# Kernel tuning notes

Measured on AMD Instinct MI355X. Metric: run time of the kernel, lower is better.

The kernel has to match this reference:

```python
import jax, jax.numpy as jnp
import numpy as np

EPS = 1e-5  # forward() default eps


def setup_inputs() -> dict:
    key = jax.random.key(0)
    k1, k2 = jax.random.split(key)
    x = jax.random.normal(k1, (16, 4, 1024, 1024), dtype=jnp.float32)
    hole = jax.random.uniform(k2, x.shape) < 0.3
    x = jnp.where(hole, 0.0, x)
    return {"x": x}


def reference(x):
    # mask_type='eq', mask_value=0: valid positions are x != 0
    valid = x != 0.0
    v = valid.astype(x.dtype)
    axes = (1, 2, 3)  # per-sample reduction over C,H,W (4D input skips per-channel branch)
    n = jnp.sum(v, axis=axes, keepdims=True)                       # [B,1,1,1] valid counts
    mean = jnp.sum(x * v, axis=axes, keepdims=True) / n            # masked mean
    centered = jnp.where(valid, x - mean, x)                       # masked-out entries unchanged
    # torch.var on the masked subset of the centered values: unbiased (ddof=1)
    m2 = jnp.sum(centered * v, axis=axes, keepdims=True) / n
    var = jnp.sum(v * (centered - m2) ** 2, axis=axes, keepdims=True) / (n - 1.0)
    out = jnp.where(valid, centered / (jnp.sqrt(var) + EPS), x)
    return out
```

## Files before the change

kernel.cpp:

```cpp
#include <hip/hip_runtime.h>


#define EPS 1e-5

typedef float v4f __attribute__((ext_vector_type(4)));

constexpr int B               = 16;
constexpr int VEC_PER_SAMPLE  = 1 << 20;
constexpr int RED_BLOCKS_PS   = 128;
constexpr int RED_THREADS     = 256;
constexpr int RED_VPT         = VEC_PER_SAMPLE / (RED_BLOCKS_PS * RED_THREADS);
constexpr int NORM_THREADS    = 256;
constexpr int NORM_VPT        = 4;
constexpr int NORM_BLOCKS_PS  = VEC_PER_SAMPLE / (NORM_THREADS * NORM_VPT);

constexpr size_t FIN_OFFSET = (size_t)B * RED_BLOCKS_PS * 3 * sizeof(double);

__global__ __launch_bounds__(RED_THREADS)
void masked_stats_kernel(const float4* __restrict__ x, double* __restrict__ part) {
    const int sample = blockIdx.x / RED_BLOCKS_PS;
    const int blk    = blockIdx.x % RED_BLOCKS_PS;
    const float4* xs = x + (size_t)sample * VEC_PER_SAMPLE
                         + (size_t)blk * (RED_THREADS * RED_VPT);

    float s1[4] = {0.f, 0.f, 0.f, 0.f};
    float s2[4] = {0.f, 0.f, 0.f, 0.f};
    int   cn[4] = {0, 0, 0, 0};

    for (int k = 0; k < RED_VPT; k += 4) {
        #pragma unroll
        for (int u = 0; u < 4; ++u) {
            float4 v = xs[(k + u) * RED_THREADS + threadIdx.x];
            s1[u] += (v.x + v.y) + (v.z + v.w);
            s2[u] += v.x * v.x;
            s2[u] += v.y * v.y;
            s2[u] += v.z * v.z;
            s2[u] += v.w * v.w;
            cn[u] += (v.x != 0.0f) + (v.y != 0.0f) + (v.z != 0.0f) + (v.w != 0.0f);
        }
    }

    double d1 = ((double)s1[0] + s1[1]) + ((double)s1[2] + s1[3]);
    double d2 = ((double)s2[0] + s2[1]) + ((double)s2[2] + s2[3]);
    int    ct = (cn[0] + cn[1]) + (cn[2] + cn[3]);

    #pragma unroll
    for (int off = 32; off > 0; off >>= 1) {
        d1 += __shfl_down(d1, off);
        d2 += __shfl_down(d2, off);
        ct += __shfl_down(ct, off);
    }

    __shared__ double L1[4], L2[4];
    __shared__ int    LC[4];
    const int wave = threadIdx.x >> 6;
    if ((threadIdx.x & 63) == 0) { L1[wave] = d1; L2[wave] = d2; LC[wave] = ct; }
    __syncthreads();
    if (threadIdx.x == 0) {
        double t1 = 0.0, t2 = 0.0; int tc = 0;
        #pragma unroll
        for (int w = 0; w < 4; ++w) { t1 += L1[w]; t2 += L2[w]; tc += LC[w]; }
        part[(size_t)blockIdx.x * 3 + 0] = t1;
        part[(size_t)blockIdx.x * 3 + 1] = t2;
        part[(size_t)blockIdx.x * 3 + 2] = (double)tc;
    }
}

__global__ __launch_bounds__(128)
void finalize_stats_kernel(const double* __restrict__ part, float2* __restrict__ fin) {
    const int sample = blockIdx.x;
    const size_t p = ((size_t)sample * RED_BLOCKS_PS + threadIdx.x) * 3;
    double d1 = part[p + 0];
    double d2 = part[p + 1];
    double dc = part[p + 2];

    #pragma unroll
    for (int off = 32; off > 0; off >>= 1) {
        d1 += __shfl_down(d1, off);
        d2 += __shfl_down(d2, off);
        dc += __shfl_down(dc, off);
    }

    __shared__ double L1[2], L2[2], LC[2];
    const int wave = threadIdx.x >> 6;
    if ((threadIdx.x & 63) == 0) { L1[wave] = d1; L2[wave] = d2; LC[wave] = dc; }
    __syncthreads();
    if (threadIdx.x == 0) {
        double S1 = L1[0] + L1[1];
        double S2 = L2[0] + L2[1];
        double n  = LC[0] + LC[1];
        double mean = S1 / n;
        double var  = (S2 - S1 * S1 / n) / (n - 1.0);
        float2 mi;
        mi.x = (float)mean;
        mi.y = (float)(1.0 / (sqrt(var) + EPS));
        fin[sample] = mi;
    }
}

__global__ __launch_bounds__(NORM_THREADS)
void masked_norm_kernel(const float4* __restrict__ x, v4f* __restrict__ out,
                        const float2* __restrict__ fin) {
    const int sample = blockIdx.x / NORM_BLOCKS_PS;
    const int blk    = blockIdx.x % NORM_BLOCKS_PS;
    const float2 mi  = fin[sample];
    const float mean = mi.x, inv = mi.y;

    const size_t base = (size_t)sample * VEC_PER_SAMPLE
                      + (size_t)blk * (NORM_THREADS * NORM_VPT);

    #pragma unroll
    for (int u = 0; u < NORM_VPT; ++u) {
        const size_t idx = base + (size_t)u * NORM_THREADS + threadIdx.x;
        float4 v = x[idx];
        v4f o;
        o.x = (v.x != 0.0f) ? (v.x - mean) * inv : 0.0f;
        o.y = (v.y != 0.0f) ? (v.y - mean) * inv : 0.0f;
        o.z = (v.z != 0.0f) ? (v.z - mean) * inv : 0.0f;
        o.w = (v.w != 0.0f) ? (v.w - mean) * inv : 0.0f;
        __builtin_nontemporal_store(o, &out[idx]);
    }
}

extern "C" void kernel_launch(void* const* d_in, const int* in_sizes, int n_in,
                              void* d_out, int out_size, void* d_ws, size_t ws_size,
                              hipStream_t stream) {
    const float4* x    = (const float4*)d_in[0];
    v4f*          out  = (v4f*)d_out;
    double*       part = (double*)d_ws;
    float2*       fin  = (float2*)((char*)d_ws + FIN_OFFSET);

    masked_stats_kernel<<<B * RED_BLOCKS_PS, RED_THREADS, 0, stream>>>(x, part);
    finalize_stats_kernel<<<B, 128, 0, stream>>>(part, fin);
    masked_norm_kernel<<<B * NORM_BLOCKS_PS, NORM_THREADS, 0, stream>>>(x, out, fin);
}
```

Before: 473.8 us.

## Fuse stats, finalize and normalize into one cooperative kernel with grid sync

Replaces the three-kernel pipeline with a single cooperative kernel. Each block computes partial sums and publishes them with release stores, then a grid-wide sync runs. After the sync each block reduces its sample's partials and normalizes the same chunk it just read. This removes two kernel launches and the intermediate finalize step, and may reuse cached input. In exchange it needs all blocks co-resident and pays a grid barrier.

```diff
diff --git a/kernel.cpp b/kernel.cpp
--- a/kernel.cpp
+++ b/kernel.cpp
@@ -1,36 +1,35 @@
 #include <hip/hip_runtime.h>
+#include <hip/hip_cooperative_groups.h>
 
 
 #define EPS 1e-5
 
 typedef float v4f __attribute__((ext_vector_type(4)));
 
-constexpr int B               = 16;
-constexpr int VEC_PER_SAMPLE  = 1 << 20;
-constexpr int RED_BLOCKS_PS   = 128;
-constexpr int RED_THREADS     = 256;
-constexpr int RED_VPT         = VEC_PER_SAMPLE / (RED_BLOCKS_PS * RED_THREADS);
-constexpr int NORM_THREADS    = 256;
-constexpr int NORM_VPT        = 4;
-constexpr int NORM_BLOCKS_PS  = VEC_PER_SAMPLE / (NORM_THREADS * NORM_VPT);
+constexpr int B              = 16;
+constexpr int VEC_PER_SAMPLE = 1 << 20;
+constexpr int THREADS        = 256;
+constexpr int BLOCKS_PS      = 64;
+constexpr int BLOCKS         = B * BLOCKS_PS;
+constexpr int VPT            = VEC_PER_SAMPLE / (BLOCKS_PS * THREADS);
 
-constexpr size_t FIN_OFFSET = (size_t)B * RED_BLOCKS_PS * 3 * sizeof(double);
-
-__global__ __launch_bounds__(RED_THREADS)
-void masked_stats_kernel(const float4* __restrict__ x, double* __restrict__ part) {
-    const int sample = blockIdx.x / RED_BLOCKS_PS;
-    const int blk    = blockIdx.x % RED_BLOCKS_PS;
-    const float4* xs = x + (size_t)sample * VEC_PER_SAMPLE
-                         + (size_t)blk * (RED_THREADS * RED_VPT);
+__global__ __launch_bounds__(THREADS, 4)
+void fused_masked_norm(const float4* __restrict__ x, v4f* __restrict__ out,
+                       double* __restrict__ part) {
+    const int sample = blockIdx.x / BLOCKS_PS;
+    const int blk    = blockIdx.x % BLOCKS_PS;
+    const size_t base = (size_t)sample * VEC_PER_SAMPLE
+                      + (size_t)blk * (THREADS * VPT);
+    const float4* xs = x + base;
 
     float s1[4] = {0.f, 0.f, 0.f, 0.f};
     float s2[4] = {0.f, 0.f, 0.f, 0.f};
     int   cn[4] = {0, 0, 0, 0};
 
-    for (int k = 0; k < RED_VPT; k += 4) {
+    for (int k = 0; k < VPT; k += 4) {
         #pragma unroll
         for (int u = 0; u < 4; ++u) {
-            float4 v = xs[(k + u) * RED_THREADS + threadIdx.x];
+            float4 v = xs[(k + u) * THREADS + threadIdx.x];
             s1[u] += (v.x + v.y) + (v.z + v.w);
             s2[u] += v.x * v.x;
             s2[u] += v.y * v.y;
@@ -57,68 +56,55 @@
     if ((threadIdx.x & 63) == 0) { L1[wave] = d1; L2[wave] = d2; LC[wave] = ct; }
     __syncthreads();
     if (threadIdx.x == 0) {
-        double t1 = 0.0, t2 = 0.0; int tc = 0;
-        #pragma unroll
-        for (int w = 0; w < 4; ++w) { t1 += L1[w]; t2 += L2[w]; tc += LC[w]; }
-        part[(size_t)blockIdx.x * 3 + 0] = t1;
-        part[(size_t)blockIdx.x * 3 + 1] = t2;
-        part[(size_t)blockIdx.x * 3 + 2] = (double)tc;
-    }
-}
-
-__global__ __launch_bounds__(128)
-void finalize_stats_kernel(const double* __restrict__ part, float2* __restrict__ fin) {
-    const int sample = blockIdx.x;
-    const size_t p = ((size_t)sample * RED_BLOCKS_PS + threadIdx.x) * 3;
-    double d1 = part[p + 0];
-    double d2 = part[p + 1];
-    double dc = part[p + 2];
-
-    #pragma unroll
-    for (int off = 32; off > 0; off >>= 1) {
-        d1 += __shfl_down(d1, off);
-        d2 += __shfl_down(d2, off);
-        dc += __shfl_down(dc, off);
+        double t1 = (L1[0] + L1[1]) + (L1[2] + L1[3]);
+        double t2 = (L2[0] + L2[1]) + (L2[2] + L2[3]);
+        double tc = (double)((LC[0] + LC[1]) + (LC[2] + LC[3]));
+        __hip_atomic_store(&part[(size_t)blockIdx.x * 3 + 0], t1,
+                           __ATOMIC_RELEASE, __HIP_MEMORY_SCOPE_AGENT);
+        __hip_atomic_store(&part[(size_t)blockIdx.x * 3 + 1], t2,
+                           __ATOMIC_RELEASE, __HIP_MEMORY_SCOPE_AGENT);
+        __hip_atomic_store(&part[(size_t)blockIdx.x * 3 + 2], tc,
+                           __ATOMIC_RELEASE, __HIP_MEMORY_SCOPE_AGENT);
     }
 
-    __shared__ double L1[2], L2[2], LC[2];
-    const int wave = threadIdx.x >> 6;
-    if ((threadIdx.x & 63) == 0) { L1[wave] = d1; L2[wave] = d2; LC[wave] = dc; }
+    cooperative_groups::this_grid().sync();
+
+    __shared__ float SMEAN, SINV;
+    if (threadIdx.x < 64) {
+        const size_t p = ((size_t)sample * BLOCKS_PS + threadIdx.x) * 3;
+        double e1 = __hip_atomic_load(&part[p + 0], __ATOMIC_ACQUIRE, __HIP_MEMORY_SCOPE_AGENT);
+        double e2 = __hip_atomic_load(&part[p + 1], __ATOMIC_ACQUIRE, __HIP_MEMORY_SCOPE_AGENT);
+        double ec = __hip_atomic_load(&part[p + 2], __ATOMIC_ACQUIRE, __HIP_MEMORY_SCOPE_AGENT);
+        #pragma unroll
+        for (int off = 32; off > 0; off >>= 1) {
+            e1 += __shfl_down(e1, off);
+            e2 += __shfl_down(e2, off);
+            ec += __shfl_down(ec, off);
+        }
+        if (threadIdx.x == 0) {
+            double n    = ec;
+            double mean = e1 / n;
+            double var  = (e2 - e1 * e1 / n) / (n - 1.0);
+            SMEAN = (float)mean;
+            SINV  = (float)(1.0 / (sqrt(var) + EPS));
+        }
+    }
     __syncthreads();
-    if (threadIdx.x == 0) {
-        double S1 = L1[0] + L1[1];
-        double S2 = L2[0] + L2[1];
-        double n  = LC[0] + LC[1];
-        double mean = S1 / n;
-        double var  = (S2 - S1 * S1 / n) / (n - 1.0);
-        float2 mi;
-        mi.x = (float)mean;
-        mi.y = (float)(1.0 / (sqrt(var) + EPS));
-        fin[sample] = mi;
-    }
-}
+    const float mean = SMEAN;
+    const float inv  = SINV;
 
-__global__ __launch_bounds__(NORM_THREADS)
-void masked_norm_kernel(const float4* __restrict__ x, v4f* __restrict__ out,
-                        const float2* __restrict__ fin) {
-    const int sample = blockIdx.x / NORM_BLOCKS_PS;
-    const int blk    = blockIdx.x % NORM_BLOCKS_PS;
-    const float2 mi  = fin[sample];
-    const float mean = mi.x, inv = mi.y;
-
-    const size_t base = (size_t)sample * VEC_PER_SAMPLE
-                      + (size_t)blk * (NORM_THREADS * NORM_VPT);
-
-    #pragma unroll
-    for (int u = 0; u < NORM_VPT; ++u) {
-        const size_t idx = base + (size_t)u * NORM_THREADS + threadIdx.x;
-        float4 v = x[idx];
-        v4f o;
-        o.x = (v.x != 0.0f) ? (v.x - mean) * inv : 0.0f;
-        o.y = (v.y != 0.0f) ? (v.y - mean) * inv : 0.0f;
-        o.z = (v.z != 0.0f) ? (v.z - mean) * inv : 0.0f;
-        o.w = (v.w != 0.0f) ? (v.w - mean) * inv : 0.0f;
-        __builtin_nontemporal_store(o, &out[idx]);
+    for (int k = 0; k < VPT; k += 4) {
+        #pragma unroll
+        for (int u = 0; u < 4; ++u) {
+            const size_t idx = base + (size_t)(k + u) * THREADS + threadIdx.x;
+            float4 v = x[idx];
+            v4f o;
+            o.x = (v.x != 0.0f) ? (v.x - mean) * inv : 0.0f;
+            o.y = (v.y != 0.0f) ? (v.y - mean) * inv : 0.0f;
+            o.z = (v.z != 0.0f) ? (v.z - mean) * inv : 0.0f;
+            o.w = (v.w != 0.0f) ? (v.w - mean) * inv : 0.0f;
+            __builtin_nontemporal_store(o, &out[idx]);
+        }
     }
 }
 
@@ -128,9 +114,8 @@
     const float4* x    = (const float4*)d_in[0];
     v4f*          out  = (v4f*)d_out;
     double*       part = (double*)d_ws;
-    float2*       fin  = (float2*)((char*)d_ws + FIN_OFFSET);
 
-    masked_stats_kernel<<<B * RED_BLOCKS_PS, RED_THREADS, 0, stream>>>(x, part);
-    finalize_stats_kernel<<<B, 128, 0, stream>>>(part, fin);
-    masked_norm_kernel<<<B * NORM_BLOCKS_PS, NORM_THREADS, 0, stream>>>(x, out, fin);
+    void* args[] = { (void*)&x, (void*)&out, (void*)&part };
+    hipLaunchCooperativeKernel(reinterpret_cast<void*>(fused_masked_norm),
+                               dim3(BLOCKS), dim3(THREADS), args, 0, stream);
 }
```

After: 705.8 us. 1.49x slower.
